# Kernel optimization log

Hardware: AMD Instinct MI355X
Metric: run time of the kernel (lower is better)

## Reference

```python
import jax, jax.numpy as jnp
import numpy as np

B, C, H, W = 4, 64, 64, 64
INTER = 16  # in_c // k


def setup_inputs() -> dict:
    key = jax.random.key(0)
    ks = jax.random.split(key, 12)
    sC = 1.0 / np.sqrt(C)
    sI = 1.0 / np.sqrt(INTER)
    return {
        "x":   jax.random.normal(ks[0], (B, C, H, W), dtype=jnp.float32),
        "Wq":  jax.random.normal(ks[1], (INTER, C), dtype=jnp.float32) * sC,
        "bq":  jax.random.normal(ks[2], (INTER,), dtype=jnp.float32) * 0.1,
        "Wk":  jax.random.normal(ks[3], (INTER, C), dtype=jnp.float32) * sC,
        "bk":  jax.random.normal(ks[4], (INTER,), dtype=jnp.float32) * 0.1,
        "wcq": jax.random.normal(ks[5], (INTER,), dtype=jnp.float32) * sI,
        "wck": jax.random.normal(ks[6], (INTER,), dtype=jnp.float32) * sI,
        "Wv":  jax.random.normal(ks[7], (C, C), dtype=jnp.float32) * sC,
        "bv":  jax.random.normal(ks[8], (C,), dtype=jnp.float32) * 0.1,
        "Wg":  jax.random.normal(ks[9], (C, C), dtype=jnp.float32) * sC,
        "bg":  jax.random.normal(ks[10], (C,), dtype=jnp.float32) * 0.1,
    }


def reference(x, Wq, bq, Wk, bk, wcq, wck, Wv, bv, Wg, bg):
    b_, c_, h_, w_ = x.shape
    n = h_ * w_
    xf = x.reshape(b_, c_, n)  # (B, C, N)
    # 1x1 conv projections (per-pixel linear maps)
    q = jnp.einsum('oc,bcn->bon', Wq, xf) + bq[None, :, None]  # (B, inter, N)
    k = jnp.einsum('oc,bcn->bon', Wk, xf) + bk[None, :, None]  # (B, inter, N)
    # concat_conv (1x1, no bias) over [q_i ; k_j] decomposes into an outer sum:
    # energy[b,i,j] = wcq . q[b,:,i] + wck . k[b,:,j]
    a = jnp.einsum('o,bon->bn', wcq, q)  # (B, N)
    d = jnp.einsum('o,bon->bn', wck, k)  # (B, N)
    energy = jax.nn.elu(a[:, :, None] + d[:, None, :])  # (B, N, N)
    energy = energy / (1.5 * jnp.sum(energy, axis=1, keepdims=True))
    v = jnp.einsum('oc,bcn->bon', Wv, xf) + bv[None, :, None]  # (B, C, N)
    out = jnp.einsum('bci,bij->bcj', v, energy)  # (B, C, N)
    # gamma 1x1 conv
    out = jnp.einsum('oc,bcn->bon', Wg, out) + bg[None, :, None]
    return out.reshape(b_, c_, h_, w_)
```

## Files before the change

### kernel.cpp

```cpp
#include <hip/hip_runtime.h>
#include <math.h>

#define NB 4096

#define LEAFo  0
#define MASTo  768
#define RELo   864
#define GHo    1120
#define GCNTo  17504
#define MEMSET_BYTES 135552
#define Do     33888
#define VGo    50272
#define ASo    1098848
#define PERMo  1115232
#define BSTo   1131616
#define Po     1148000
#define PSEAo  1197152
#define PSAo   1197408

__device__ __forceinline__ void gst(float* p, float v) {
    __hip_atomic_store(p, v, __ATOMIC_RELAXED, __HIP_MEMORY_SCOPE_AGENT);
}
__device__ __forceinline__ void gsti(int* p, int v) {
    __hip_atomic_store(p, v, __ATOMIC_RELAXED, __HIP_MEMORY_SCOPE_AGENT);
}

__device__ __forceinline__ int bucket_of(float v) {
    int k = (int)((v + 16.0f) * 128.0f);
    k = k < 0 ? 0 : k;
    k = k > (NB - 1) ? (NB - 1) : k;
    return k;
}

__device__ __forceinline__ void gbar(int* wsi, int idx) {
    __syncthreads();
    if (threadIdx.x == 0) {
        int leaf = blockIdx.x & 7;
        bool bcast = false;
        int old = __hip_atomic_fetch_add(wsi + LEAFo + (idx * 8 + leaf) * 32, 1,
                                         __ATOMIC_RELAXED, __HIP_MEMORY_SCOPE_AGENT);
        if (old == 31) {
            int m = __hip_atomic_fetch_add(wsi + MASTo + idx * 32, 1,
                                           __ATOMIC_RELAXED, __HIP_MEMORY_SCOPE_AGENT);
            if (m == 7) {
#pragma unroll
                for (int i = 0; i < 8; i++)
                    __hip_atomic_store(wsi + RELo + i * 32, idx + 1,
                                       __ATOMIC_RELAXED, __HIP_MEMORY_SCOPE_AGENT);
                bcast = true;
            }
        }
        if (!bcast) {
            const int* myrel = wsi + RELo + leaf * 32;
            while (__hip_atomic_load(myrel, __ATOMIC_RELAXED, __HIP_MEMORY_SCOPE_AGENT) <= idx)
                __builtin_amdgcn_s_sleep(8);
        }
    }
    __syncthreads();
}

__global__ __launch_bounds__(256, 1) void k_fused(
        const float* __restrict__ x,
        const float* __restrict__ Wq, const float* __restrict__ bq,
        const float* __restrict__ Wk, const float* __restrict__ bk,
        const float* __restrict__ wcq, const float* __restrict__ wck,
        const float* __restrict__ Wv, const float* __restrict__ bv,
        const float* __restrict__ Wg, const float* __restrict__ bg,
        float* __restrict__ ws, float* __restrict__ out) {
    __shared__ float smem[13056];
    int tid = threadIdx.x;
    int bid = blockIdx.x;
    int b = bid >> 6, t6 = bid & 63;
    int* wsi = (int*)ws;
    int* gh  = wsi + GHo;

    float myA = 0.f;

    {
        float* xt  = smem;
        float* wt  = smem + 4608;
        float* wqe = smem + 9216, *wke = smem + 9280, *bvg = smem + 9344, *misc = smem + 9408;
        if (tid < 64) {
            float s1 = 0.f, s2 = 0.f, s3 = 0.f;
            for (int o = 0; o < 16; o++) { s1 += wcq[o] * Wq[o * 64 + tid]; s2 += wck[o] * Wk[o * 64 + tid]; }
            for (int m = 0; m < 64; m++) s3 += Wg[tid * 64 + m] * bv[m];
            wqe[tid] = s1; wke[tid] = s2; bvg[tid] = s3;
        } else if (tid == 64) {
            float s = 0.f; for (int o = 0; o < 16; o++) s += wcq[o] * bq[o]; misc[0] = s;
        } else if (tid == 65) {
            float s = 0.f; for (int o = 0; o < 16; o++) s += wck[o] * bk[o]; misc[1] = s;
        }
        {
            int o = tid & 63, c0 = (tid >> 6) * 16;
            float acc[16];
#pragma unroll
            for (int k = 0; k < 16; k++) acc[k] = 0.f;
            for (int m = 0; m < 64; m++) {
                float wg = Wg[o * 64 + m];
                const float4* wv4 = (const float4*)(Wv + m * 64 + c0);
                float4 a0 = wv4[0], a1 = wv4[1], a2 = wv4[2], a3 = wv4[3];
                acc[0] += wg * a0.x; acc[1] += wg * a0.y; acc[2] += wg * a0.z; acc[3] += wg * a0.w;
                acc[4] += wg * a1.x; acc[5] += wg * a1.y; acc[6] += wg * a1.z; acc[7] += wg * a1.w;
                acc[8] += wg * a2.x; acc[9] += wg * a2.y; acc[10] += wg * a2.z; acc[11] += wg * a2.w;
                acc[12] += wg * a3.x; acc[13] += wg * a3.y; acc[14] += wg * a3.z; acc[15] += wg * a3.w;
            }
#pragma unroll
            for (int k = 0; k < 16; k++) wt[(c0 + k) * 72 + o] = acc[k];
        }
        const float4* xb4 = (const float4*)(x + (size_t)b * 64 * 4096);
#pragma unroll
        for (int idx = tid; idx < 1024; idx += 256) {
            int c = idx >> 4, nl4 = idx & 15;
            *(float4*)&xt[c * 72 + nl4 * 4] = xb4[c * 1024 + t6 * 16 + nl4];
        }
        __syncthreads();
        if (tid < 64) {
            float s1 = misc[0], s2 = misc[1];
            for (int c = 0; c < 64; c++) {
                float xv = xt[c * 72 + tid];
                s1 += wqe[c] * xv; s2 += wke[c] * xv;
            }
            myA = s1;
            ws[Do + b * 4096 + t6 * 64 + tid] = s2;
            atomicAdd(&gh[b * 4096 + bucket_of(s1)], 1);
        }
        {
            int o = tid & 63, nl0 = (tid >> 6) * 16;
            float acc[16];
            float bo = bvg[o];
#pragma unroll
            for (int k = 0; k < 16; k++) acc[k] = bo;
            for (int c = 0; c < 64; c++) {
                float wv = wt[c * 72 + o];
                const float* xr = &xt[c * 72 + nl0];
#pragma unroll
                for (int k = 0; k < 16; k++) acc[k] += wv * xr[k];
            }
#pragma unroll
            for (int k = 0; k < 16; k++)
                gst(&ws[VGo + ((size_t)(b * 4096) + t6 * 64 + nl0 + k) * 64 + o], acc[k]);
        }
    }
    gbar(wsi, 0);

    {
        unsigned int* hist = (unsigned int*)smem;
        unsigned int* wtot = hist + 4096;
        const int* gh_b = gh + b * 4096;
        int* gcnt = wsi + GCNTo + b * 4096;
#pragma unroll 4
        for (int i = tid; i < NB; i += 256) hist[i] = (unsigned int)gh_b[i];
        __syncthreads();
        int lane = tid & 63, w = tid >> 6;
        unsigned int s = 0u; int base = tid * 16;
#pragma unroll
        for (int k = 0; k < 16; k++) s += hist[base + k];
        unsigned int inc = s;
        for (int off = 1; off < 64; off <<= 1) {
            unsigned int u = __shfl_up(inc, off);
            if (lane >= off) inc += u;
        }
        if (lane == 63) wtot[w] = inc;
        __syncthreads();
        unsigned int run = inc - s;
        for (int w2 = 0; w2 < w; w2++) run += wtot[w2];
        for (int k = 0; k < 16; k++) {
            unsigned int h = hist[base + k];
            hist[base + k] = run;
            run += h;
        }
        __syncthreads();
        if (t6 == 0) {
            int* bst = wsi + BSTo;
#pragma unroll 4
            for (int i = tid; i < NB; i += 256) gsti(&bst[b * 4096 + i], (int)hist[i]);
        }
        if (tid < 64) {
            int i = t6 * 64 + tid;
            int kb = bucket_of(myA);
            int r = (int)hist[kb] + atomicAdd(&gcnt[kb], 1);
            gst(&ws[ASo + b * 4096 + r], myA);
            gsti((int*)ws + PERMo + b * 4096 + r, i);
        }
    }
    gbar(wsi, 1);

    {
        int c = tid & 63, w = tid >> 6;
        int r0 = t6 * 64 + w * 16;
        const int* perm = (const int*)ws + PERMo;
        int pk[16]; float avs[16], wvs[16];
#pragma unroll
        for (int k = 0; k < 16; k++) pk[k] = perm[b * 4096 + r0 + k];
#pragma unroll
        for (int k = 0; k < 16; k++) avs[k] = ws[ASo + b * 4096 + r0 + k];
#pragma unroll
        for (int k = 0; k < 16; k++) wvs[k] = ws[VGo + ((size_t)(b * 4096) + pk[k]) * 64 + c];
        float s1 = 0.f, s2 = 0.f, s3 = 0.f, sea_w = 0.f, sa_w = 0.f;
#pragma unroll
        for (int k = 0; k < 16; k++) {
            float ea = expf(avs[k]);
            s1 += wvs[k]; s2 += wvs[k] * ea; s3 += wvs[k] * avs[k];
            sea_w += ea; sa_w += avs[k];
        }
        float* partL = smem;
        float* wsc   = smem + 768;
        partL[(w * 3 + 0) * 64 + c] = s1;
        partL[(w * 3 + 1) * 64 + c] = s2;
        partL[(w * 3 + 2) * 64 + c] = s3;
        if (c == 0) { wsc[w] = sea_w; wsc[4 + w] = sa_w; }
        __syncthreads();
        if (tid < 192) {
            int g = tid >> 6, cc = tid & 63;
            float s = partL[(0 * 3 + g) * 64 + cc] + partL[(1 * 3 + g) * 64 + cc]
                    + partL[(2 * 3 + g) * 64 + cc] + partL[(3 * 3 + g) * 64 + cc];
            gst(&ws[Po + (b * 64 + t6) * 192 + tid], s);
        } else if (tid == 192) {
            gst(&ws[PSEAo + b * 64 + t6], wsc[0] + wsc[1] + wsc[2] + wsc[3]);
            gst(&ws[PSAo  + b * 64 + t6], wsc[4] + wsc[5] + wsc[6] + wsc[7]);
        }
    }
    gbar(wsi, 2);

    {
        float* CP     = smem;
        float* cpsea  = smem + 12545;
        float* cpsa   = smem + 12610;
        float* djs    = smem + 12675;
        float* edjs   = smem + 12739;
        float* invden = smem + 12803;
        int*   qarr   = (int*)(smem + 12867);
        float* bgs    = smem + 12931;
        if (tid < 192) {
            float v[64];
#pragma unroll
            for (int ch = 0; ch < 64; ch++) v[ch] = ws[Po + b * 12288 + ch * 192 + tid];
            float r = 0.f;
#pragma unroll
            for (int q = 0; q < 64; q++) { CP[q * 193 + tid] = r; r += v[q]; }
            CP[64 * 193 + tid] = r;
        } else if (tid == 192) {
            float v[64];
#pragma unroll
            for (int ch = 0; ch < 64; ch++) v[ch] = ws[PSEAo + b * 64 + ch];
            float r = 0.f;
#pragma unroll
            for (int q = 0; q < 64; q++) { cpsea[q] = r; r += v[q]; }
            cpsea[64] = r;
        } else if (tid == 193) {
            float v[64];
#pragma unroll
            for (int ch = 0; ch < 64; ch++) v[ch] = ws[PSAo + b * 64 + ch];
            float r = 0.f;
#pragma unroll
            for (int q = 0; q < 64; q++) { cpsa[q] = r; r += v[q]; }
            cpsa[64] = r;
        } else if (tid >= 194 && tid < 258) {
        }
        if (tid >= 194 - 64 && tid < 194) { }
        if (tid < 64) bgs[tid] = bg[tid];
        __syncthreads();
        const int* bst = (const int*)ws + BSTo;
        int j0 = t6 * 64;
        if (tid < 64) {
            int j = j0 + tid;
            float dj = ws[Do + b * 4096 + j];
            float edj = expf(dj);
            int kb = bucket_of(-dj);
            int t = bst[b * NB + kb];
            int q = (t + 32) >> 6;
            float den = 1.5f * ((cpsa[64] - cpsa[q]) + dj * (float)(4096 - 64 * q)
                                - (float)(64 * q) + edj * cpsea[q]);
            qarr[tid] = q; djs[tid] = dj; edjs[tid] = edj; invden[tid] = 1.0f / den;
        }
        __syncthreads();
        {
            int jl = tid & 63, cq = tid >> 6;
            float dj = djs[jl], edj = edjs[jl], inv = invden[jl];
            int qb = qarr[jl] * 193;
            for (int cc = cq; cc < 64; cc += 4) {
                float c1 = CP[qb + cc], c2 = CP[qb + 64 + cc], c3 = CP[qb + 128 + cc];
                float t1 = CP[64 * 193 + cc], t3 = CP[64 * 193 + 128 + cc];
                float num = (t3 - c3) + dj * t1 - (1.0f + dj) * c1 + edj * c2;
                out[((size_t)(b * 64 + cc)) * 4096 + j0 + jl] = num * inv + bgs[cc];
            }
        }
    }
}

extern "C" void kernel_launch(void* const* d_in, const int* in_sizes, int n_in,
                              void* d_out, int out_size, void* d_ws, size_t ws_size,
                              hipStream_t stream) {
    const float* x   = (const float*)d_in[0];
    const float* Wq  = (const float*)d_in[1];
    const float* bq  = (const float*)d_in[2];
    const float* Wk  = (const float*)d_in[3];
    const float* bk  = (const float*)d_in[4];
    const float* wcq = (const float*)d_in[5];
    const float* wck = (const float*)d_in[6];
    const float* Wv  = (const float*)d_in[7];
    const float* bv  = (const float*)d_in[8];
    const float* Wg  = (const float*)d_in[9];
    const float* bg  = (const float*)d_in[10];
    float* ws  = (float*)d_ws;
    float* out = (float*)d_out;

    hipMemsetAsync(d_ws, 0, MEMSET_BYTES, stream);
    k_fused<<<256, 256, 0, stream>>>(x, Wq, bq, Wk, bk, wcq, wck, Wv, bv, Wg, bg, ws, out);
}
```

Before: 107.2 us.

## Widen fused kernel to 1024 threads per block and parallelize prefix scans

Raises the block size from 256 to 1024 threads. Each phase is re-partitioned so every thread does a quarter of the former work: fewer accumulators in the weight-fold and projection loops, a 4-element histogram scan, 16 segments in the gather reduction, and the column prefix sums split into 4 segments combined through a shared-memory segment-total pass. The aim is to shorten the serial per-thread work, especially the 64-long prefix loops run by only 194 threads. In exchange it adds extra syncs and a second shared-memory pass, and the sleep in the grid-barrier spin loop is also shortened.

```diff
diff --git a/kernel.cpp b/kernel.cpp
--- a/kernel.cpp
+++ b/kernel.cpp
@@ -53,13 +53,13 @@
         if (!bcast) {
             const int* myrel = wsi + RELo + leaf * 32;
             while (__hip_atomic_load(myrel, __ATOMIC_RELAXED, __HIP_MEMORY_SCOPE_AGENT) <= idx)
-                __builtin_amdgcn_s_sleep(8);
+                __builtin_amdgcn_s_sleep(4);
         }
     }
     __syncthreads();
 }
 
-__global__ __launch_bounds__(256, 1) void k_fused(
+__global__ __launch_bounds__(1024, 1) void k_fused(
         const float* __restrict__ x,
         const float* __restrict__ Wq, const float* __restrict__ bq,
         const float* __restrict__ Wk, const float* __restrict__ bk,
@@ -67,7 +67,7 @@
         const float* __restrict__ Wv, const float* __restrict__ bv,
         const float* __restrict__ Wg, const float* __restrict__ bg,
         float* __restrict__ ws, float* __restrict__ out) {
-    __shared__ float smem[13056];
+    __shared__ float smem[13824];
     int tid = threadIdx.x;
     int bid = blockIdx.x;
     int b = bid >> 6, t6 = bid & 63;
@@ -91,26 +91,19 @@
             float s = 0.f; for (int o = 0; o < 16; o++) s += wck[o] * bk[o]; misc[1] = s;
         }
         {
-            int o = tid & 63, c0 = (tid >> 6) * 16;
-            float acc[16];
-#pragma unroll
-            for (int k = 0; k < 16; k++) acc[k] = 0.f;
+            int o = tid & 63, c0 = (tid >> 6) * 4;
+            float a0 = 0.f, a1 = 0.f, a2 = 0.f, a3 = 0.f;
             for (int m = 0; m < 64; m++) {
                 float wg = Wg[o * 64 + m];
-                const float4* wv4 = (const float4*)(Wv + m * 64 + c0);
-                float4 a0 = wv4[0], a1 = wv4[1], a2 = wv4[2], a3 = wv4[3];
-                acc[0] += wg * a0.x; acc[1] += wg * a0.y; acc[2] += wg * a0.z; acc[3] += wg * a0.w;
-                acc[4] += wg * a1.x; acc[5] += wg * a1.y; acc[6] += wg * a1.z; acc[7] += wg * a1.w;
-                acc[8] += wg * a2.x; acc[9] += wg * a2.y; acc[10] += wg * a2.z; acc[11] += wg * a2.w;
-                acc[12] += wg * a3.x; acc[13] += wg * a3.y; acc[14] += wg * a3.z; acc[15] += wg * a3.w;
-            }
-#pragma unroll
-            for (int k = 0; k < 16; k++) wt[(c0 + k) * 72 + o] = acc[k];
-        }
-        const float4* xb4 = (const float4*)(x + (size_t)b * 64 * 4096);
-#pragma unroll
-        for (int idx = tid; idx < 1024; idx += 256) {
-            int c = idx >> 4, nl4 = idx & 15;
+                const float4 wv4 = *(const float4*)(Wv + m * 64 + c0);
+                a0 += wg * wv4.x; a1 += wg * wv4.y; a2 += wg * wv4.z; a3 += wg * wv4.w;
+            }
+            wt[(c0 + 0) * 72 + o] = a0; wt[(c0 + 1) * 72 + o] = a1;
+            wt[(c0 + 2) * 72 + o] = a2; wt[(c0 + 3) * 72 + o] = a3;
+        }
+        {
+            const float4* xb4 = (const float4*)(x + (size_t)b * 64 * 4096);
+            int c = tid >> 4, nl4 = tid & 15;
             *(float4*)&xt[c * 72 + nl4 * 4] = xb4[c * 1024 + t6 * 16 + nl4];
         }
         __syncthreads();
@@ -125,20 +118,19 @@
             atomicAdd(&gh[b * 4096 + bucket_of(s1)], 1);
         }
         {
-            int o = tid & 63, nl0 = (tid >> 6) * 16;
-            float acc[16];
+            int o = tid & 63, nl0 = (tid >> 6) * 4;
             float bo = bvg[o];
-#pragma unroll
-            for (int k = 0; k < 16; k++) acc[k] = bo;
+            float a0 = bo, a1 = bo, a2 = bo, a3 = bo;
             for (int c = 0; c < 64; c++) {
                 float wv = wt[c * 72 + o];
                 const float* xr = &xt[c * 72 + nl0];
-#pragma unroll
-                for (int k = 0; k < 16; k++) acc[k] += wv * xr[k];
-            }
-#pragma unroll
-            for (int k = 0; k < 16; k++)
-                gst(&ws[VGo + ((size_t)(b * 4096) + t6 * 64 + nl0 + k) * 64 + o], acc[k]);
+                a0 += wv * xr[0]; a1 += wv * xr[1]; a2 += wv * xr[2]; a3 += wv * xr[3];
+            }
+            size_t base = ((size_t)(b * 4096) + t6 * 64 + nl0) * 64 + o;
+            gst(&ws[VGo + base], a0);
+            gst(&ws[VGo + base + 64], a1);
+            gst(&ws[VGo + base + 128], a2);
+            gst(&ws[VGo + base + 192], a3);
         }
     }
     gbar(wsi, 0);
@@ -148,13 +140,13 @@
         unsigned int* wtot = hist + 4096;
         const int* gh_b = gh + b * 4096;
         int* gcnt = wsi + GCNTo + b * 4096;
-#pragma unroll 4
-        for (int i = tid; i < NB; i += 256) hist[i] = (unsigned int)gh_b[i];
+#pragma unroll
+        for (int i = tid; i < NB; i += 1024) hist[i] = (unsigned int)gh_b[i];
         __syncthreads();
         int lane = tid & 63, w = tid >> 6;
-        unsigned int s = 0u; int base = tid * 16;
-#pragma unroll
-        for (int k = 0; k < 16; k++) s += hist[base + k];
+        int base = tid * 4;
+        unsigned int h0 = hist[base], h1 = hist[base + 1], h2 = hist[base + 2], h3 = hist[base + 3];
+        unsigned int s = h0 + h1 + h2 + h3;
         unsigned int inc = s;
         for (int off = 1; off < 64; off <<= 1) {
             unsigned int u = __shfl_up(inc, off);
@@ -164,16 +156,15 @@
         __syncthreads();
         unsigned int run = inc - s;
         for (int w2 = 0; w2 < w; w2++) run += wtot[w2];
-        for (int k = 0; k < 16; k++) {
-            unsigned int h = hist[base + k];
-            hist[base + k] = run;
-            run += h;
-        }
+        hist[base] = run; run += h0;
+        hist[base + 1] = run; run += h1;
+        hist[base + 2] = run; run += h2;
+        hist[base + 3] = run;
         __syncthreads();
         if (t6 == 0) {
             int* bst = wsi + BSTo;
-#pragma unroll 4
-            for (int i = tid; i < NB; i += 256) gsti(&bst[b * 4096 + i], (int)hist[i]);
+#pragma unroll
+            for (int i = tid; i < NB; i += 1024) gsti(&bst[b * 4096 + i], (int)hist[i]);
         }
         if (tid < 64) {
             int i = t6 * 64 + tid;
@@ -186,79 +177,100 @@
     gbar(wsi, 1);
 
     {
-        int c = tid & 63, w = tid >> 6;
-        int r0 = t6 * 64 + w * 16;
+        int c = tid & 63, seg = tid >> 6;
+        int r0 = t6 * 64 + seg * 4;
         const int* perm = (const int*)ws + PERMo;
-        int pk[16]; float avs[16], wvs[16];
-#pragma unroll
-        for (int k = 0; k < 16; k++) pk[k] = perm[b * 4096 + r0 + k];
-#pragma unroll
-        for (int k = 0; k < 16; k++) avs[k] = ws[ASo + b * 4096 + r0 + k];
-#pragma unroll
-        for (int k = 0; k < 16; k++) wvs[k] = ws[VGo + ((size_t)(b * 4096) + pk[k]) * 64 + c];
+        int pk[4]; float avs[4], wvs[4];
+#pragma unroll
+        for (int k = 0; k < 4; k++) pk[k] = perm[b * 4096 + r0 + k];
+#pragma unroll
+        for (int k = 0; k < 4; k++) avs[k] = ws[ASo + b * 4096 + r0 + k];
+#pragma unroll
+        for (int k = 0; k < 4; k++) wvs[k] = ws[VGo + ((size_t)(b * 4096) + pk[k]) * 64 + c];
         float s1 = 0.f, s2 = 0.f, s3 = 0.f, sea_w = 0.f, sa_w = 0.f;
 #pragma unroll
-        for (int k = 0; k < 16; k++) {
+        for (int k = 0; k < 4; k++) {
             float ea = expf(avs[k]);
             s1 += wvs[k]; s2 += wvs[k] * ea; s3 += wvs[k] * avs[k];
             sea_w += ea; sa_w += avs[k];
         }
         float* partL = smem;
-        float* wsc   = smem + 768;
-        partL[(w * 3 + 0) * 64 + c] = s1;
-        partL[(w * 3 + 1) * 64 + c] = s2;
-        partL[(w * 3 + 2) * 64 + c] = s3;
-        if (c == 0) { wsc[w] = sea_w; wsc[4 + w] = sa_w; }
+        float* wsc   = smem + 3072;
+        partL[(seg * 3 + 0) * 64 + c] = s1;
+        partL[(seg * 3 + 1) * 64 + c] = s2;
+        partL[(seg * 3 + 2) * 64 + c] = s3;
+        if (c == 0) { wsc[seg] = sea_w; wsc[16 + seg] = sa_w; }
         __syncthreads();
         if (tid < 192) {
             int g = tid >> 6, cc = tid & 63;
-            float s = partL[(0 * 3 + g) * 64 + cc] + partL[(1 * 3 + g) * 64 + cc]
-                    + partL[(2 * 3 + g) * 64 + cc] + partL[(3 * 3 + g) * 64 + cc];
+            float s = 0.f;
+#pragma unroll
+            for (int sg = 0; sg < 16; sg++) s += partL[(sg * 3 + g) * 64 + cc];
             gst(&ws[Po + (b * 64 + t6) * 192 + tid], s);
         } else if (tid == 192) {
-            gst(&ws[PSEAo + b * 64 + t6], wsc[0] + wsc[1] + wsc[2] + wsc[3]);
-            gst(&ws[PSAo  + b * 64 + t6], wsc[4] + wsc[5] + wsc[6] + wsc[7]);
+            float s = 0.f;
+#pragma unroll
+            for (int sg = 0; sg < 16; sg++) s += wsc[sg];
+            gst(&ws[PSEAo + b * 64 + t6], s);
+        } else if (tid == 193) {
+            float s = 0.f;
+#pragma unroll
+            for (int sg = 0; sg < 16; sg++) s += wsc[16 + sg];
+            gst(&ws[PSAo + b * 64 + t6], s);
         }
     }
     gbar(wsi, 2);
 
     {
         float* CP     = smem;
-        float* cpsea  = smem + 12545;
-        float* cpsa   = smem + 12610;
-        float* djs    = smem + 12675;
-        float* edjs   = smem + 12739;
-        float* invden = smem + 12803;
-        int*   qarr   = (int*)(smem + 12867);
-        float* bgs    = smem + 12931;
-        if (tid < 192) {
-            float v[64];
-#pragma unroll
-            for (int ch = 0; ch < 64; ch++) v[ch] = ws[Po + b * 12288 + ch * 192 + tid];
+        float* segtot = smem + 12545;
+        float* scseg  = smem + 13313;
+        float* cpsea  = smem + 13321;
+        float* cpsa   = smem + 13386;
+        float* djs    = smem + 13451;
+        float* edjs   = smem + 13515;
+        float* invden = smem + 13579;
+        int*   qarr   = (int*)(smem + 13643);
+        float* bgs    = smem + 13707;
+        float v[16]; int col = 0, seg = 0;
+        if (tid < 768) {
+            col = tid % 192; seg = tid / 192;
+            float s = 0.f;
+#pragma unroll
+            for (int u = 0; u < 16; u++) {
+                v[u] = ws[Po + b * 12288 + (seg * 16 + u) * 192 + col];
+                s += v[u];
+            }
+            segtot[seg * 192 + col] = s;
+        } else if (tid < 776) {
+            int idx = tid - 768; int which = idx & 1; seg = idx >> 1;
+            const float* src = which ? &ws[PSAo + b * 64] : &ws[PSEAo + b * 64];
+            float s = 0.f;
+#pragma unroll
+            for (int u = 0; u < 16; u++) { v[u] = src[seg * 16 + u]; s += v[u]; }
+            scseg[which * 4 + seg] = s;
+        } else if (tid < 840) {
+            bgs[tid - 776] = bg[tid - 776];
+        }
+        __syncthreads();
+        if (tid < 768) {
             float r = 0.f;
-#pragma unroll
-            for (int q = 0; q < 64; q++) { CP[q * 193 + tid] = r; r += v[q]; }
-            CP[64 * 193 + tid] = r;
-        } else if (tid == 192) {
-            float v[64];
-#pragma unroll
-            for (int ch = 0; ch < 64; ch++) v[ch] = ws[PSEAo + b * 64 + ch];
+            for (int s2 = 0; s2 < seg; s2++) r += segtot[s2 * 192 + col];
+#pragma unroll
+            for (int u = 0; u < 16; u++) {
+                CP[(seg * 16 + u) * 193 + col] = r;
+                r += v[u];
+            }
+            if (seg == 3) CP[64 * 193 + col] = r;
+        } else if (tid < 776) {
+            int idx = tid - 768; int which = idx & 1; seg = idx >> 1;
+            float* dst = which ? cpsa : cpsea;
             float r = 0.f;
-#pragma unroll
-            for (int q = 0; q < 64; q++) { cpsea[q] = r; r += v[q]; }
-            cpsea[64] = r;
-        } else if (tid == 193) {
-            float v[64];
-#pragma unroll
-            for (int ch = 0; ch < 64; ch++) v[ch] = ws[PSAo + b * 64 + ch];
-            float r = 0.f;
-#pragma unroll
-            for (int q = 0; q < 64; q++) { cpsa[q] = r; r += v[q]; }
-            cpsa[64] = r;
-        } else if (tid >= 194 && tid < 258) {
-        }
-        if (tid >= 194 - 64 && tid < 194) { }
-        if (tid < 64) bgs[tid] = bg[tid];
+            for (int s2 = 0; s2 < seg; s2++) r += scseg[which * 4 + s2];
+#pragma unroll
+            for (int u = 0; u < 16; u++) { dst[seg * 16 + u] = r; r += v[u]; }
+            if (seg == 3) dst[64] = r;
+        }
         __syncthreads();
         const int* bst = (const int*)ws + BSTo;
         int j0 = t6 * 64;
@@ -278,7 +290,8 @@
             int jl = tid & 63, cq = tid >> 6;
             float dj = djs[jl], edj = edjs[jl], inv = invden[jl];
             int qb = qarr[jl] * 193;
-            for (int cc = cq; cc < 64; cc += 4) {
+#pragma unroll
+            for (int cc = cq; cc < 64; cc += 16) {
                 float c1 = CP[qb + cc], c2 = CP[qb + 64 + cc], c3 = CP[qb + 128 + cc];
                 float t1 = CP[64 * 193 + cc], t3 = CP[64 * 193 + 128 + cc];
                 float num = (t3 - c3) + dj * t1 - (1.0f + dj) * c1 + edj * c2;
@@ -306,5 +319,5 @@
     float* out = (float*)d_out;
 
     hipMemsetAsync(d_ws, 0, MEMSET_BYTES, stream);
-    k_fused<<<256, 256, 0, stream>>>(x, Wq, bq, Wk, bk, wcq, wck, Wv, bv, Wg, bg, ws, out);
-}
+    k_fused<<<256, 1024, 0, stream>>>(x, Wq, bq, Wk, bk, wcq, wck, Wv, bv, Wg, bg, ws, out);
+}
```

Measured after the change: 109.7 us. 1.02x slower.

## Keep per-pixel d and bucket rank in registers, pack counters into histogram

Applied to the files above, without the earlier changes.

The d projection and its bucket-start rank now stay in registers across grid barriers, so the global D array and the bucket-start table with their round trips are removed. The scatter counter is packed into the upper 16 bits of the histogram word, which removes the separate count array and shrinks the workspace memset. The x tile loads are issued early and Wg is transposed through shared memory so it is read coalesced. The barrier spin sleep is shortened. These changes trade extra shared memory and a 16-bit packing limit for less global traffic and lower barrier latency.

```diff
diff --git a/kernel.cpp b/kernel.cpp
--- a/kernel.cpp
+++ b/kernel.cpp
@@ -7,16 +7,13 @@
 #define MASTo  768
 #define RELo   864
 #define GHo    1120
-#define GCNTo  17504
-#define MEMSET_BYTES 135552
-#define Do     33888
-#define VGo    50272
-#define ASo    1098848
-#define PERMo  1115232
-#define BSTo   1131616
-#define Po     1148000
-#define PSEAo  1197152
-#define PSAo   1197408
+#define MEMSET_BYTES 70016
+#define VGo    17504
+#define ASo    1066080
+#define PERMo  1082464
+#define Po     1098848
+#define PSEAo  1148000
+#define PSAo   1148256
 
 __device__ __forceinline__ void gst(float* p, float v) {
     __hip_atomic_store(p, v, __ATOMIC_RELAXED, __HIP_MEMORY_SCOPE_AGENT);
@@ -53,7 +50,7 @@
         if (!bcast) {
             const int* myrel = wsi + RELo + leaf * 32;
             while (__hip_atomic_load(myrel, __ATOMIC_RELAXED, __HIP_MEMORY_SCOPE_AGENT) <= idx)
-                __builtin_amdgcn_s_sleep(8);
+                __builtin_amdgcn_s_sleep(1);
         }
     }
     __syncthreads();
@@ -67,19 +64,38 @@
         const float* __restrict__ Wv, const float* __restrict__ bv,
         const float* __restrict__ Wg, const float* __restrict__ bg,
         float* __restrict__ ws, float* __restrict__ out) {
-    __shared__ float smem[13056];
+    __shared__ float smem[13824];
     int tid = threadIdx.x;
     int bid = blockIdx.x;
     int b = bid >> 6, t6 = bid & 63;
     int* wsi = (int*)ws;
-    int* gh  = wsi + GHo;
-
-    float myA = 0.f;
+
+    float myA = 0.f, myD = 0.f;
+    int   myQ = 0;
 
     {
         float* xt  = smem;
         float* wt  = smem + 4608;
-        float* wqe = smem + 9216, *wke = smem + 9280, *bvg = smem + 9344, *misc = smem + 9408;
+        float* wgT = smem + 9216;
+        float* wqe = smem + 13312, *wke = smem + 13376, *bvg = smem + 13440, *misc = smem + 13504;
+        const float4* xb4 = (const float4*)(x + (size_t)b * 64 * 4096);
+        float4 xr[4];
+#pragma unroll
+        for (int k = 0; k < 4; k++) {
+            int idx = tid + k * 256, c = idx >> 4, nl4 = idx & 15;
+            xr[k] = xb4[c * 1024 + t6 * 16 + nl4];
+        }
+        {
+            const float4* wg4 = (const float4*)Wg;
+            int o = tid >> 2;
+#pragma unroll
+            for (int k4 = 0; k4 < 4; k4++) {
+                float4 g = wg4[tid * 4 + k4];
+                int m0 = (tid & 3) * 16 + k4 * 4;
+                wgT[(m0 + 0) * 64 + o] = g.x; wgT[(m0 + 1) * 64 + o] = g.y;
+                wgT[(m0 + 2) * 64 + o] = g.z; wgT[(m0 + 3) * 64 + o] = g.w;
+            }
+        }
         if (tid < 64) {
             float s1 = 0.f, s2 = 0.f, s3 = 0.f;
             for (int o = 0; o < 16; o++) { s1 += wcq[o] * Wq[o * 64 + tid]; s2 += wck[o] * Wk[o * 64 + tid]; }
@@ -90,13 +106,19 @@
         } else if (tid == 65) {
             float s = 0.f; for (int o = 0; o < 16; o++) s += wck[o] * bk[o]; misc[1] = s;
         }
+#pragma unroll
+        for (int k = 0; k < 4; k++) {
+            int idx = tid + k * 256, c = idx >> 4, nl4 = idx & 15;
+            *(float4*)&xt[c * 72 + nl4 * 4] = xr[k];
+        }
+        __syncthreads();
         {
             int o = tid & 63, c0 = (tid >> 6) * 16;
             float acc[16];
 #pragma unroll
             for (int k = 0; k < 16; k++) acc[k] = 0.f;
             for (int m = 0; m < 64; m++) {
-                float wg = Wg[o * 64 + m];
+                float wg = wgT[m * 64 + o];
                 const float4* wv4 = (const float4*)(Wv + m * 64 + c0);
                 float4 a0 = wv4[0], a1 = wv4[1], a2 = wv4[2], a3 = wv4[3];
                 acc[0] += wg * a0.x; acc[1] += wg * a0.y; acc[2] += wg * a0.z; acc[3] += wg * a0.w;
@@ -107,12 +129,6 @@
 #pragma unroll
             for (int k = 0; k < 16; k++) wt[(c0 + k) * 72 + o] = acc[k];
         }
-        const float4* xb4 = (const float4*)(x + (size_t)b * 64 * 4096);
-#pragma unroll
-        for (int idx = tid; idx < 1024; idx += 256) {
-            int c = idx >> 4, nl4 = idx & 15;
-            *(float4*)&xt[c * 72 + nl4 * 4] = xb4[c * 1024 + t6 * 16 + nl4];
-        }
         __syncthreads();
         if (tid < 64) {
             float s1 = misc[0], s2 = misc[1];
@@ -120,9 +136,8 @@
                 float xv = xt[c * 72 + tid];
                 s1 += wqe[c] * xv; s2 += wke[c] * xv;
             }
-            myA = s1;
-            ws[Do + b * 4096 + t6 * 64 + tid] = s2;
-            atomicAdd(&gh[b * 4096 + bucket_of(s1)], 1);
+            myA = s1; myD = s2;
+            atomicAdd(&wsi[GHo + b * 4096 + bucket_of(s1)], 1);
         }
         {
             int o = tid & 63, nl0 = (tid >> 6) * 16;
@@ -132,9 +147,9 @@
             for (int k = 0; k < 16; k++) acc[k] = bo;
             for (int c = 0; c < 64; c++) {
                 float wv = wt[c * 72 + o];
-                const float* xr = &xt[c * 72 + nl0];
-#pragma unroll
-                for (int k = 0; k < 16; k++) acc[k] += wv * xr[k];
+                const float* xr2 = &xt[c * 72 + nl0];
+#pragma unroll
+                for (int k = 0; k < 16; k++) acc[k] += wv * xr2[k];
             }
 #pragma unroll
             for (int k = 0; k < 16; k++)
@@ -146,10 +161,9 @@
     {
         unsigned int* hist = (unsigned int*)smem;
         unsigned int* wtot = hist + 4096;
-        const int* gh_b = gh + b * 4096;
-        int* gcnt = wsi + GCNTo + b * 4096;
+        int* gh_b = wsi + GHo + b * 4096;
 #pragma unroll 4
-        for (int i = tid; i < NB; i += 256) hist[i] = (unsigned int)gh_b[i];
+        for (int i = tid; i < NB; i += 256) hist[i] = (unsigned int)gh_b[i] & 0xFFFFu;
         __syncthreads();
         int lane = tid & 63, w = tid >> 6;
         unsigned int s = 0u; int base = tid * 16;
@@ -170,15 +184,12 @@
             run += h;
         }
         __syncthreads();
-        if (t6 == 0) {
-            int* bst = wsi + BSTo;
-#pragma unroll 4
-            for (int i = tid; i < NB; i += 256) gsti(&bst[b * 4096 + i], (int)hist[i]);
-        }
         if (tid < 64) {
+            myQ = ((int)hist[bucket_of(-myD)] + 32) >> 6;
             int i = t6 * 64 + tid;
             int kb = bucket_of(myA);
-            int r = (int)hist[kb] + atomicAdd(&gcnt[kb], 1);
+            int old = atomicAdd(&gh_b[kb], 0x10000);
+            int r = (int)hist[kb] + (old >> 16);
             gst(&ws[ASo + b * 4096 + r], myA);
             gsti((int*)ws + PERMo + b * 4096 + r, i);
         }
@@ -217,7 +228,8 @@
             gst(&ws[Po + (b * 64 + t6) * 192 + tid], s);
         } else if (tid == 192) {
             gst(&ws[PSEAo + b * 64 + t6], wsc[0] + wsc[1] + wsc[2] + wsc[3]);
-            gst(&ws[PSAo  + b * 64 + t6], wsc[4] + wsc[5] + wsc[6] + wsc[7]);
+        } else if (tid == 193) {
+            gst(&ws[PSAo + b * 64 + t6], wsc[4] + wsc[5] + wsc[6] + wsc[7]);
         }
     }
     gbar(wsi, 2);
@@ -255,20 +267,14 @@
 #pragma unroll
             for (int q = 0; q < 64; q++) { cpsa[q] = r; r += v[q]; }
             cpsa[64] = r;
-        } else if (tid >= 194 && tid < 258) {
-        }
-        if (tid >= 194 - 64 && tid < 194) { }
+        }
         if (tid < 64) bgs[tid] = bg[tid];
         __syncthreads();
-        const int* bst = (const int*)ws + BSTo;
         int j0 = t6 * 64;
         if (tid < 64) {
-            int j = j0 + tid;
-            float dj = ws[Do + b * 4096 + j];
+            float dj = myD;
             float edj = expf(dj);
-            int kb = bucket_of(-dj);
-            int t = bst[b * NB + kb];
-            int q = (t + 32) >> 6;
+            int q = myQ;
             float den = 1.5f * ((cpsa[64] - cpsa[q]) + dj * (float)(4096 - 64 * q)
                                 - (float)(64 * q) + edj * cpsea[q]);
             qarr[tid] = q; djs[tid] = dj; edjs[tid] = edj; invden[tid] = 1.0f / den;
```

Result: faster. 102.8 us (-4.1%).
